# Performance work log

Measured on AMD Instinct MI355X. Metric: run time of the kernel, lower is better.

Reference implementation:

```python
import jax, jax.numpy as jnp
import numpy as np

T, B, IN, H1, HB = 512, 256, 64, 128, 32  # seq, batch, input, LSTM width, bottleneck


def _lstm(x, w_ih, w_hh, b_ih, b_hh):
    """Single-layer unidirectional LSTM, time-major x: [T,B,in] -> [T,B,H].
    PyTorch gate order: i, f, g, o. Zero initial state."""
    H = w_hh.shape[1]
    # hoist input projection out of the scan: [T,B,4H]
    xg = jnp.einsum('tbi,gi->tbg', x, w_ih) + b_ih + b_hh

    def step(carry, xt):
        h, c = carry
        g = xt + h @ w_hh.T
        i, f, gg, o = jnp.split(g, 4, axis=-1)
        c = jax.nn.sigmoid(f) * c + jax.nn.sigmoid(i) * jnp.tanh(gg)
        h = jax.nn.sigmoid(o) * jnp.tanh(c)
        return (h, c), h

    h0 = jnp.zeros((x.shape[1], H), x.dtype)
    (_, _), hs = jax.lax.scan(step, (h0, h0), xg)
    return hs


def setup_inputs() -> dict:
    key = jax.random.key(0)
    ks = jax.random.split(key, 17)
    s = 0.05

    def p(k, shape):
        return jax.random.normal(k, shape, dtype=jnp.float32) * s

    return {
        'X': jax.random.normal(ks[0], (T, B, IN), dtype=jnp.float32),
        # en1: IN -> H1
        'w1_ih': p(ks[1], (4 * H1, IN)), 'w1_hh': p(ks[2], (4 * H1, H1)),
        'b1_ih': p(ks[3], (4 * H1,)), 'b1_hh': p(ks[4], (4 * H1,)),
        # en2: H1 -> HB
        'w2_ih': p(ks[5], (4 * HB, H1)), 'w2_hh': p(ks[6], (4 * HB, HB)),
        'b2_ih': p(ks[7], (4 * HB,)), 'b2_hh': p(ks[8], (4 * HB,)),
        # de1: HB -> H1
        'w3_ih': p(ks[9], (4 * H1, HB)), 'w3_hh': p(ks[10], (4 * H1, H1)),
        'b3_ih': p(ks[11], (4 * H1,)), 'b3_hh': p(ks[12], (4 * H1,)),
        # de2: H1 -> IN
        'w4_ih': p(ks[13], (4 * IN, H1)), 'w4_hh': p(ks[14], (4 * IN, IN)),
        'b4_ih': p(ks[15], (4 * IN,)), 'b4_hh': p(ks[16], (4 * IN,)),
    }


def reference(X, w1_ih, w1_hh, b1_ih, b1_hh, w2_ih, w2_hh, b2_ih, b2_hh,
              w3_ih, w3_hh, b3_ih, b3_hh, w4_ih, w4_hh, b4_ih, b4_hh):
    h = _lstm(X, w1_ih, w1_hh, b1_ih, b1_hh)      # [T,B,128]
    h = _lstm(h, w2_ih, w2_hh, b2_ih, b2_hh)      # [T,B,32]
    h = jnp.tanh(h)                               # bottleneck tanh
    h = _lstm(h, w3_ih, w3_hh, b3_ih, b3_hh)      # [T,B,128]
    out = _lstm(h, w4_ih, w4_hh, b4_ih, b4_hh)    # [T,B,64]
    return out
```

## Files before the change

### kernel.cpp

```cpp
#include <hip/hip_runtime.h>

#define T_STEPS 512
#define BATCH   256

typedef _Float16 f16;
typedef unsigned long long u64;
typedef unsigned int u32;
typedef __attribute__((ext_vector_type(8))) _Float16 f16x8;
typedef __attribute__((ext_vector_type(4))) _Float16 f16x4;
typedef __attribute__((ext_vector_type(4))) float    f32x4;

#define L2E 1.44269504088896340736f

__device__ __forceinline__ float rcp_f(float x)  { return __builtin_amdgcn_rcpf(x); }
__device__ __forceinline__ float exp2_f(float x) { return __builtin_amdgcn_exp2f(x); }

__device__ __forceinline__ float tanh_n(float x) {
    return fmaf(-2.0f, rcp_f(1.0f + exp2_f(2.0f * L2E * x)), 1.0f);
}
__device__ __forceinline__ u64 tanh4_f16(u64 v) {
    f16x4 h = __builtin_bit_cast(f16x4, v);
    f16x4 r;
#pragma unroll
    for (int i = 0; i < 4; ++i) r[i] = (f16)tanh_n((float)h[i]);
    return __builtin_bit_cast(u64, r);
}

__device__ __forceinline__ void barrier_lgkm() {
    asm volatile("s_waitcnt lgkmcnt(0)\n\ts_barrier" ::: "memory");
}
__device__ __forceinline__ void barrier_drain() {
    asm volatile("s_waitcnt vmcnt(0) lgkmcnt(0)\n\ts_barrier" ::: "memory");
}

__device__ __forceinline__ int  flag_load(const int* p) {
    return __hip_atomic_load(p, __ATOMIC_RELAXED, __HIP_MEMORY_SCOPE_AGENT);
}
__device__ __forceinline__ void flag_store(int* p, int v) {
    __hip_atomic_store(p, v, __ATOMIC_RELAXED, __HIP_MEMORY_SCOPE_AGENT);
}
__device__ __forceinline__ u64  panel_load(const u64* p) {
    return __hip_atomic_load(p, __ATOMIC_RELAXED, __HIP_MEMORY_SCOPE_AGENT);
}
__device__ __forceinline__ void panel_store(u64* p, u64 v) {
    __hip_atomic_store(p, v, __ATOMIC_RELAXED, __HIP_MEMORY_SCOPE_AGENT);
}

__device__ __forceinline__ void cvt_store4(f16* dst, f32x4 v) {
    f16x4 h;
    h[0] = (f16)v[0]; h[1] = (f16)v[1]; h[2] = (f16)v[2]; h[3] = (f16)v[3];
    *reinterpret_cast<f16x4*>(dst) = h;
}

template <int IN_DIM, int H>
struct Lstm {
    static constexpr int KTX = IN_DIM / 32, KTH = H / 32, KT = KTX + KTH;
    f16x8 bw[4][KT];
    float bias[4];
    float cst[4];
    int u, q;

    __device__ __forceinline__ void init(const float* __restrict__ w_ih,
                                         const float* __restrict__ w_hh,
                                         const float* __restrict__ b_ih,
                                         const float* __restrict__ b_hh,
                                         int unit, int lane) {
        q = lane >> 4;
        u = unit * 16 + (lane & 15);
#pragma unroll
        for (int g = 0; g < 4; ++g) {
            const float sc = (g == 2) ? 2.0f * L2E : L2E;
            const int row = g * H + u;
#pragma unroll
            for (int kt = 0; kt < KTX; ++kt) {
                const float* p = w_ih + (size_t)row * IN_DIM + kt * 32 + q * 8;
                f16x8 v;
#pragma unroll
                for (int j = 0; j < 8; ++j) v[j] = (f16)(p[j] * sc);
                bw[g][kt] = v;
            }
#pragma unroll
            for (int kt = 0; kt < KTH; ++kt) {
                const float* p = w_hh + (size_t)row * H + kt * 32 + q * 8;
                f16x8 v;
#pragma unroll
                for (int j = 0; j < 8; ++j) v[j] = (f16)(p[j] * sc);
                bw[g][KTX + kt] = v;
            }
            bias[g] = (b_ih[g * H + u] + b_hh[g * H + u]) * sc;
            cst[g] = 0.f;
        }
    }

    __device__ __forceinline__ void step(const f16* in_row, const f16* rec_row,
                                         f16* hdst, int hp, float hold[4]) {
        f16x8 a[KT];
#pragma unroll
        for (int kt = 0; kt < KTX; ++kt)
            a[kt] = *reinterpret_cast<const f16x8*>(in_row + kt * 32 + q * 8);
#pragma unroll
        for (int kt = 0; kt < KTH; ++kt)
            a[KTX + kt] = *reinterpret_cast<const f16x8*>(rec_row + kt * 32 + q * 8);
        f32x4 acc[4];
#pragma unroll
        for (int g = 0; g < 4; ++g)
            acc[g] = (f32x4){bias[g], bias[g], bias[g], bias[g]};
#pragma unroll
        for (int kt = 0; kt < KT; ++kt)
#pragma unroll
            for (int g = 0; g < 4; ++g)
                acc[g] = __builtin_amdgcn_mfma_f32_16x16x32_f16(a[kt], bw[g][kt], acc[g], 0, 0, 0);
#pragma unroll
        for (int r = 0; r < 4; ++r) {
            const float yi = acc[0][r], yf = acc[1][r], yg = acc[2][r], yo = acc[3][r];
            const float si = rcp_f(1.0f + exp2_f(-yi));
            const float sf = rcp_f(1.0f + exp2_f(-yf));
            const float dg = rcp_f(1.0f + exp2_f(yg));
            const float tgp = fmaf(dg, -4.0f * L2E, 2.0f * L2E);
            cst[r] = fmaf(sf, cst[r], si * tgp);
            const float dc = rcp_f(1.0f + exp2_f(cst[r]));
            const float th = fmaf(-2.0f, dc, 1.0f);
            const float so = rcp_f(1.0f + exp2_f(-yo));
            const float h = so * th;
            hdst[(4 * q + r) * hp + u] = (f16)h;
            hold[r] = h;
        }
    }
};

__global__ __launch_bounds__(768, 3)
void lstm_fused(const float* __restrict__ X,
                const float* __restrict__ w1_ih, const float* __restrict__ w1_hh,
                const float* __restrict__ b1_ih, const float* __restrict__ b1_hh,
                const float* __restrict__ w2_ih, const float* __restrict__ w2_hh,
                const float* __restrict__ b2_ih, const float* __restrict__ b2_hh,
                const float* __restrict__ w3_ih, const float* __restrict__ w3_hh,
                const float* __restrict__ b3_ih, const float* __restrict__ b3_hh,
                const float* __restrict__ w4_ih, const float* __restrict__ w4_hh,
                const float* __restrict__ b4_ih, const float* __restrict__ b4_hh,
                f16* __restrict__ h2t, int* __restrict__ flags,
                float* __restrict__ out)
{
    __shared__ __attribute__((aligned(16))) char sm[16384];
    const int b = blockIdx.x, tid = threadIdx.x;
    const int wave = tid >> 6, lane = tid & 63;
    const int col = lane & 15;

    if (b < 16) {
        const int g = b, bblk = g * 16;
        int* out_flag = flags + g;
        constexpr int XP1 = 72, HP1 = 136, HP2 = 40;
        constexpr int XS_P = 16 * XP1, H1_P = 16 * HP1, H2_P = 16 * HP2;
        f16* xs  = (f16*)sm;
        f16* h1  = (f16*)(sm + 4608);
        f16* h2r = (f16*)(sm + 13312);

        for (int i = tid; i < (2 * H1_P + 2 * H2_P) / 2; i += 768)
            ((u32*)h1)[i] = 0u;

        const float* xg0 = nullptr; const float* xg1 = nullptr;
        f16* xl0 = nullptr; f16* xl1 = nullptr;
        f32x4 hv0{}, hv1{};
        if (wave >= 10) {
            const int c0 = tid - 640, c1 = c0 + 128;
            const int r0 = c0 >> 4, o0 = (c0 & 15) * 4;
            const int r1 = c1 >> 4, o1 = (c1 & 15) * 4;
            xg0 = X + (size_t)(bblk + r0) * 64 + o0;
            xg1 = X + (size_t)(bblk + r1) * 64 + o1;
            xl0 = xs + r0 * XP1 + o0;
            xl1 = xs + r1 * XP1 + o1;
            f32x4 v0 = *(const f32x4*)xg0, v1 = *(const f32x4*)xg1;
            cvt_store4(xl0, v0); cvt_store4(xl1, v1);
            xg0 += (size_t)BATCH * 64; xg1 += (size_t)BATCH * 64;
            hv0 = *(const f32x4*)xg0; hv1 = *(const f32x4*)xg1;
            xg0 += (size_t)BATCH * 64; xg1 += (size_t)BATCH * 64;
        }
        barrier_lgkm();

        if (wave < 8) {
            Lstm<64, 128> L;
            L.init(w1_ih, w1_hh, b1_ih, b1_hh, wave, lane);
            float hd[4];
            const f16* in0 = xs + col * XP1;
            const f16* in1 = xs + XS_P + col * XP1;
            const f16* rc0 = h1 + col * HP1;
            const f16* rc1 = h1 + H1_P + col * HP1;
            f16* d0 = h1;
            f16* d1 = h1 + H1_P;
            for (int ss = 0; ss < 512; ss += 2) {
                L.step(in0, rc1, d0, HP1, hd);
                barrier_lgkm();
                L.step(in1, rc0, d1, HP1, hd);
                barrier_lgkm();
            }
            barrier_lgkm();
            barrier_lgkm();
        } else if (wave < 10) {
            Lstm<128, 32> L;
            L.init(w2_ih, w2_hh, b2_ih, b2_hh, wave - 8, lane);
            float hd[4];
            const int t2id = tid - 512, orow = t2id >> 3, ooff = t2id & 7;
            u64* opg = (u64*)(h2t + (size_t)(bblk + orow) * 32) + ooff;
            const f16* in0 = h1 + col * HP1;
            const f16* in1 = h1 + H1_P + col * HP1;
            const f16* rc0 = h2r + col * HP2;
            const f16* rc1 = h2r + H2_P + col * HP2;
            f16* d0 = h2r;
            f16* d1 = h2r + H2_P;
            const f16* ol0 = h2r + orow * HP2 + ooff * 4;
            const f16* ol1 = h2r + H2_P + orow * HP2 + ooff * 4;
            for (int ss = 0; ss < 512; ss += 2) {
                if (ss >= 2) {
                    panel_store(opg, tanh4_f16(*(const u64*)ol0));
                    opg += (size_t)BATCH * 32 / 4;
                    L.step(in1, rc0, d1, HP2, hd);
                }
                if (ss >= 4 && (ss & 3) == 0) barrier_drain(); else barrier_lgkm();
                if (ss >= 4 && (ss & 3) == 0 && t2id == 0)
                    flag_store(out_flag, ss - 1);
                if (ss >= 2) {
                    panel_store(opg, tanh4_f16(*(const u64*)ol1));
                    opg += (size_t)BATCH * 32 / 4;
                }
                L.step(in0, rc1, d0, HP2, hd);
                barrier_lgkm();
            }
            panel_store(opg, tanh4_f16(*(const u64*)ol0));
            opg += (size_t)BATCH * 32 / 4;
            L.step(in1, rc0, d1, HP2, hd);
            barrier_lgkm();
            panel_store(opg, tanh4_f16(*(const u64*)ol1));
            barrier_drain();
            if (t2id == 0) flag_store(out_flag, T_STEPS + 8);
        } else {
            for (int ss = 0; ss < 512; ss += 2) {
                cvt_store4(xl0 + XS_P, hv0); cvt_store4(xl1 + XS_P, hv1);
                if (ss + 2 < 512) {
                    hv0 = *(const f32x4*)xg0; hv1 = *(const f32x4*)xg1;
                    xg0 += (size_t)BATCH * 64; xg1 += (size_t)BATCH * 64;
                }
                barrier_lgkm();
                if (ss + 2 < 512) { cvt_store4(xl0, hv0); cvt_store4(xl1, hv1); }
                if (ss + 3 < 512) {
                    hv0 = *(const f32x4*)xg0; hv1 = *(const f32x4*)xg1;
                    xg0 += (size_t)BATCH * 64; xg1 += (size_t)BATCH * 64;
                }
                barrier_lgkm();
            }
            barrier_lgkm();
            barrier_lgkm();
        }
    } else {
        const int g = b - 16, bblk = g * 16;
        const int* in_flag = flags + g;
        constexpr int XP3 = 40, HP3 = 136, HP4 = 72;
        constexpr int X3_P = 16 * XP3, H3_P = 16 * HP3, H4_P = 16 * HP4;
        f16* xs3 = (f16*)sm;
        f16* h3  = (f16*)(sm + 2560);
        f16* h4  = (f16*)(sm + 11264);

        for (int i = tid; i < (2 * H3_P + 2 * H4_P) / 2; i += 768)
            ((u32*)h3)[i] = 0u;

        const char* sgp = nullptr; f16* slp = nullptr;
        u64 ha = 0, hb = 0;
        int seen = 0;
        if (wave == 0) {
            const int r_ = tid >> 2, o_ = (tid & 3) * 8;
            sgp = (const char*)h2t + ((size_t)(bblk + r_) * 32 + o_) * 2;
            slp = xs3 + r_ * XP3 + o_;
            do { seen = flag_load(in_flag); } while (seen < 1);
            u64 pk[2];
            pk[0] = panel_load((const u64*)sgp);
            pk[1] = panel_load((const u64*)sgp + 1);
            sgp += (size_t)BATCH * 64;
            *reinterpret_cast<f16x8*>(slp) = *reinterpret_cast<const f16x8*>(pk);
            while (seen < 2) seen = flag_load(in_flag);
            ha = panel_load((const u64*)sgp);
            hb = panel_load((const u64*)sgp + 1);
            sgp += (size_t)BATCH * 64;
        }
        barrier_lgkm();

        if (wave < 8) {
            Lstm<32, 128> L;
            L.init(w3_ih, w3_hh, b3_ih, b3_hh, wave, lane);
            float hd[4];
            const f16* in0 = xs3 + col * XP3;
            const f16* in1 = xs3 + X3_P + col * XP3;
            const f16* rc0 = h3 + col * HP3;
            const f16* rc1 = h3 + H3_P + col * HP3;
            f16* d0 = h3;
            f16* d1 = h3 + H3_P;
            for (int ss = 0; ss < 512; ss += 2) {
                if (wave == 0) {
                    u64 pk[2] = {ha, hb};
                    *reinterpret_cast<f16x8*>(slp + X3_P) = *reinterpret_cast<const f16x8*>(pk);
                    if (ss + 2 < 512) {
                        if (seen < ss + 3) { do { seen = flag_load(in_flag); } while (seen < ss + 3); }
                        ha = panel_load((const u64*)sgp);
                        hb = panel_load((const u64*)sgp + 1);
                        sgp += (size_t)BATCH * 64;
                    }
                }
                L.step(in0, rc1, d0, HP3, hd);
                barrier_lgkm();
                if (wave == 0) {
                    if (ss + 2 < 512) {
                        u64 pk[2] = {ha, hb};
                        *reinterpret_cast<f16x8*>(slp) = *reinterpret_cast<const f16x8*>(pk);
                    }
                    if (ss + 3 < 512) {
                        if (seen < ss + 4) { do { seen = flag_load(in_flag); } while (seen < ss + 4); }
                        ha = panel_load((const u64*)sgp);
                        hb = panel_load((const u64*)sgp + 1);
                        sgp += (size_t)BATCH * 64;
                    }
                }
                L.step(in1, rc0, d1, HP3, hd);
                barrier_lgkm();
            }
            barrier_lgkm();
        } else {
            Lstm<128, 64> L;
            L.init(w4_ih, w4_hh, b4_ih, b4_hh, wave - 8, lane);
            float hold[4] = {0.f, 0.f, 0.f, 0.f};
            const int q4 = lane >> 4;
            const int u4 = (wave - 8) * 16 + col;
            float* outp = out + ((size_t)bblk + 4 * q4) * 64 + u4;
            const f16* in0 = h3 + col * HP3;
            const f16* in1 = h3 + H3_P + col * HP3;
            const f16* rc0 = h4 + col * HP4;
            const f16* rc1 = h4 + H4_P + col * HP4;
            f16* d0 = h4;
            f16* d1 = h4 + H4_P;
            for (int ss = 0; ss < 512; ss += 2) {
                if (ss >= 2) {
#pragma unroll
                    for (int r = 0; r < 4; ++r) outp[r * 64] = hold[r];
                    outp += (size_t)BATCH * 64;
                    L.step(in1, rc0, d1, HP4, hold);
                }
                barrier_lgkm();
                if (ss >= 2) {
#pragma unroll
                    for (int r = 0; r < 4; ++r) outp[r * 64] = hold[r];
                    outp += (size_t)BATCH * 64;
                }
                L.step(in0, rc1, d0, HP4, hold);
                barrier_lgkm();
            }
#pragma unroll
            for (int r = 0; r < 4; ++r) outp[r * 64] = hold[r];
            outp += (size_t)BATCH * 64;
            L.step(in1, rc0, d1, HP4, hold);
            barrier_lgkm();
#pragma unroll
            for (int r = 0; r < 4; ++r) outp[r * 64] = hold[r];
        }
    }
}

extern "C" void kernel_launch(void* const* d_in, const int* in_sizes, int n_in,
                              void* d_out, int out_size, void* d_ws, size_t ws_size,
                              hipStream_t stream) {
    const float* X     = (const float*)d_in[0];
    const float* w1_ih = (const float*)d_in[1];
    const float* w1_hh = (const float*)d_in[2];
    const float* b1_ih = (const float*)d_in[3];
    const float* b1_hh = (const float*)d_in[4];
    const float* w2_ih = (const float*)d_in[5];
    const float* w2_hh = (const float*)d_in[6];
    const float* b2_ih = (const float*)d_in[7];
    const float* b2_hh = (const float*)d_in[8];
    const float* w3_ih = (const float*)d_in[9];
    const float* w3_hh = (const float*)d_in[10];
    const float* b3_ih = (const float*)d_in[11];
    const float* b3_hh = (const float*)d_in[12];
    const float* w4_ih = (const float*)d_in[13];
    const float* w4_hh = (const float*)d_in[14];
    const float* b4_ih = (const float*)d_in[15];
    const float* b4_hh = (const float*)d_in[16];

    float* out = (float*)d_out;

    int* flags = (int*)d_ws;
    f16* h2t = (f16*)((char*)d_ws + 256);

    lstm_fused<<<32, 768, 0, stream>>>(X,
        w1_ih, w1_hh, b1_ih, b1_hh, w2_ih, w2_hh, b2_ih, b2_hh,
        w3_ih, w3_hh, b3_ih, b3_hh, w4_ih, w4_hh, b4_ih, b4_hh,
        h2t, flags, out);
}
```

Baseline: 721.1 us.

## Deepen cross-block prefetch pipeline, relax flag waits, and simplify gate math

The producer blocks now wait only for older vector stores (vmcnt(2)) before publishing a step flag, and publish a flag that lags by two more steps. The consumer blocks and the X loaders each prefetch one extra timestep into registers, so global loads and flag polling have more slack behind the recurrent chain. The gate nonlinearities are rewritten to share reciprocals (sigmoid*tanh computed with one rcp), and s_setprio raises wave priority during the MFMA and activation section. The deeper pipeline adds registers and more in-flight loads, and it depends on the flag lag matching the extra prefetch depth.

```diff
diff --git a/kernel.cpp b/kernel.cpp
--- a/kernel.cpp
+++ b/kernel.cpp
@@ -31,6 +31,9 @@
 }
 __device__ __forceinline__ void barrier_drain() {
     asm volatile("s_waitcnt vmcnt(0) lgkmcnt(0)\n\ts_barrier" ::: "memory");
+}
+__device__ __forceinline__ void wait_vm2() {
+    asm volatile("s_waitcnt vmcnt(2)" ::: "memory");
 }
 
 __device__ __forceinline__ int  flag_load(const int* p) {
@@ -105,6 +108,7 @@
 #pragma unroll
         for (int g = 0; g < 4; ++g)
             acc[g] = (f32x4){bias[g], bias[g], bias[g], bias[g]};
+        __builtin_amdgcn_s_setprio(1);
 #pragma unroll
         for (int kt = 0; kt < KT; ++kt)
 #pragma unroll
@@ -113,18 +117,20 @@
 #pragma unroll
         for (int r = 0; r < 4; ++r) {
             const float yi = acc[0][r], yf = acc[1][r], yg = acc[2][r], yo = acc[3][r];
-            const float si = rcp_f(1.0f + exp2_f(-yi));
-            const float sf = rcp_f(1.0f + exp2_f(-yf));
-            const float dg = rcp_f(1.0f + exp2_f(yg));
-            const float tgp = fmaf(dg, -4.0f * L2E, 2.0f * L2E);
-            cst[r] = fmaf(sf, cst[r], si * tgp);
-            const float dc = rcp_f(1.0f + exp2_f(cst[r]));
-            const float th = fmaf(-2.0f, dc, 1.0f);
-            const float so = rcp_f(1.0f + exp2_f(-yo));
-            const float h = so * th;
+            const float Ei = exp2_f(-yi);
+            const float G  = exp2_f(yg);
+            const float Ef = exp2_f(-yf);
+            const float sf = rcp_f(1.0f + Ef);
+            const float itg = (2.0f * L2E) * (G - 1.0f) *
+                              rcp_f((1.0f + Ei) * (G + 1.0f));
+            cst[r] = fmaf(sf, cst[r], itg);
+            const float C  = exp2_f(cst[r]);
+            const float Eo = exp2_f(-yo);
+            const float h  = (C - 1.0f) * rcp_f((1.0f + Eo) * (C + 1.0f));
             hdst[(4 * q + r) * hp + u] = (f16)h;
             hold[r] = h;
         }
+        __builtin_amdgcn_s_setprio(0);
     }
 };
 
@@ -160,7 +166,7 @@
 
         const float* xg0 = nullptr; const float* xg1 = nullptr;
         f16* xl0 = nullptr; f16* xl1 = nullptr;
-        f32x4 hv0{}, hv1{};
+        f32x4 hvA0{}, hvA1{}, hvB0{}, hvB1{};
         if (wave >= 10) {
             const int c0 = tid - 640, c1 = c0 + 128;
             const int r0 = c0 >> 4, o0 = (c0 & 15) * 4;
@@ -172,7 +178,9 @@
             f32x4 v0 = *(const f32x4*)xg0, v1 = *(const f32x4*)xg1;
             cvt_store4(xl0, v0); cvt_store4(xl1, v1);
             xg0 += (size_t)BATCH * 64; xg1 += (size_t)BATCH * 64;
-            hv0 = *(const f32x4*)xg0; hv1 = *(const f32x4*)xg1;
+            hvA0 = *(const f32x4*)xg0; hvA1 = *(const f32x4*)xg1;
+            xg0 += (size_t)BATCH * 64; xg1 += (size_t)BATCH * 64;
+            hvB0 = *(const f32x4*)xg0; hvB1 = *(const f32x4*)xg1;
             xg0 += (size_t)BATCH * 64; xg1 += (size_t)BATCH * 64;
         }
         barrier_lgkm();
@@ -215,9 +223,10 @@
                     opg += (size_t)BATCH * 32 / 4;
                     L.step(in1, rc0, d1, HP2, hd);
                 }
-                if (ss >= 4 && (ss & 3) == 0) barrier_drain(); else barrier_lgkm();
+                if (ss >= 4 && (ss & 3) == 0) wait_vm2();
+                barrier_lgkm();
                 if (ss >= 4 && (ss & 3) == 0 && t2id == 0)
-                    flag_store(out_flag, ss - 1);
+                    flag_store(out_flag, ss - 3);
                 if (ss >= 2) {
                     panel_store(opg, tanh4_f16(*(const u64*)ol1));
                     opg += (size_t)BATCH * 32 / 4;
@@ -234,15 +243,15 @@
             if (t2id == 0) flag_store(out_flag, T_STEPS + 8);
         } else {
             for (int ss = 0; ss < 512; ss += 2) {
-                cvt_store4(xl0 + XS_P, hv0); cvt_store4(xl1 + XS_P, hv1);
-                if (ss + 2 < 512) {
-                    hv0 = *(const f32x4*)xg0; hv1 = *(const f32x4*)xg1;
+                cvt_store4(xl0 + XS_P, hvA0); cvt_store4(xl1 + XS_P, hvA1);
+                if (ss + 3 < 512) {
+                    hvA0 = *(const f32x4*)xg0; hvA1 = *(const f32x4*)xg1;
                     xg0 += (size_t)BATCH * 64; xg1 += (size_t)BATCH * 64;
                 }
                 barrier_lgkm();
-                if (ss + 2 < 512) { cvt_store4(xl0, hv0); cvt_store4(xl1, hv1); }
-                if (ss + 3 < 512) {
-                    hv0 = *(const f32x4*)xg0; hv1 = *(const f32x4*)xg1;
+                if (ss + 2 < 512) { cvt_store4(xl0, hvB0); cvt_store4(xl1, hvB1); }
+                if (ss + 4 < 512) {
+                    hvB0 = *(const f32x4*)xg0; hvB1 = *(const f32x4*)xg1;
                     xg0 += (size_t)BATCH * 64; xg1 += (size_t)BATCH * 64;
                 }
                 barrier_lgkm();
@@ -263,8 +272,8 @@
             ((u32*)h3)[i] = 0u;
 
         const char* sgp = nullptr; f16* slp = nullptr;
-        u64 ha = 0, hb = 0;
-        int seen = 0;
+        u64 hA0 = 0, hA1 = 0, hB0 = 0, hB1 = 0;
+        int seen = 0, flp = 0;
         if (wave == 0) {
             const int r_ = tid >> 2, o_ = (tid & 3) * 8;
             sgp = (const char*)h2t + ((size_t)(bblk + r_) * 32 + o_) * 2;
@@ -276,9 +285,14 @@
             sgp += (size_t)BATCH * 64;
             *reinterpret_cast<f16x8*>(slp) = *reinterpret_cast<const f16x8*>(pk);
             while (seen < 2) seen = flag_load(in_flag);
-            ha = panel_load((const u64*)sgp);
-            hb = panel_load((const u64*)sgp + 1);
+            hA0 = panel_load((const u64*)sgp);
+            hA1 = panel_load((const u64*)sgp + 1);
             sgp += (size_t)BATCH * 64;
+            while (seen < 3) seen = flag_load(in_flag);
+            hB0 = panel_load((const u64*)sgp);
+            hB1 = panel_load((const u64*)sgp + 1);
+            sgp += (size_t)BATCH * 64;
+            flp = seen;
         }
         barrier_lgkm();
 
@@ -294,28 +308,32 @@
             f16* d1 = h3 + H3_P;
             for (int ss = 0; ss < 512; ss += 2) {
                 if (wave == 0) {
-                    u64 pk[2] = {ha, hb};
+                    u64 pk[2] = {hA0, hA1};
                     *reinterpret_cast<f16x8*>(slp + X3_P) = *reinterpret_cast<const f16x8*>(pk);
-                    if (ss + 2 < 512) {
-                        if (seen < ss + 3) { do { seen = flag_load(in_flag); } while (seen < ss + 3); }
-                        ha = panel_load((const u64*)sgp);
-                        hb = panel_load((const u64*)sgp + 1);
+                    if (ss + 3 < 512) {
+                        if (flp > seen) seen = flp;
+                        while (seen < ss + 4) seen = flag_load(in_flag);
+                        hA0 = panel_load((const u64*)sgp);
+                        hA1 = panel_load((const u64*)sgp + 1);
                         sgp += (size_t)BATCH * 64;
                     }
+                    flp = flag_load(in_flag);
                 }
                 L.step(in0, rc1, d0, HP3, hd);
                 barrier_lgkm();
                 if (wave == 0) {
                     if (ss + 2 < 512) {
-                        u64 pk[2] = {ha, hb};
+                        u64 pk[2] = {hB0, hB1};
                         *reinterpret_cast<f16x8*>(slp) = *reinterpret_cast<const f16x8*>(pk);
                     }
-                    if (ss + 3 < 512) {
-                        if (seen < ss + 4) { do { seen = flag_load(in_flag); } while (seen < ss + 4); }
-                        ha = panel_load((const u64*)sgp);
-                        hb = panel_load((const u64*)sgp + 1);
+                    if (ss + 4 < 512) {
+                        if (flp > seen) seen = flp;
+                        while (seen < ss + 5) seen = flag_load(in_flag);
+                        hB0 = panel_load((const u64*)sgp);
+                        hB1 = panel_load((const u64*)sgp + 1);
                         sgp += (size_t)BATCH * 64;
                     }
+                    flp = flag_load(in_flag);
                 }
                 L.step(in1, rc0, d1, HP3, hd);
                 barrier_lgkm();
```

Measured after the change: 695.8 us. 1.04x faster.
